# Optimization experiments

Measured on AMD Instinct MI355X. Metric: run time of the kernel, lower is better.

The kernel has to match this reference:

```python
import jax, jax.numpy as jnp
import numpy as np

N, H, D = 4, 8, 256          # num_layers, num_heads, hid_dim
DK = D // H                  # 32
DFF = D * 2                  # 512
B, L = 4, 2048               # batch, max_len


def _init_proj(key, shape):
    # matches torch init: uniform(-scale, scale), scale = sqrt(6/(fan_in+fan_out))
    s = float(np.sqrt(6.0 / (shape[-1] + shape[-2])))
    return jax.random.uniform(key, shape, jnp.float32, -s, s)


def setup_inputs() -> dict:
    key = jax.random.key(0)
    ks = jax.random.split(key, 8)
    x = jax.random.normal(ks[0], (B, L, D), jnp.float32)
    mask = (jax.random.uniform(ks[1], (B, L)) < 0.9).astype(jnp.float32)
    return {
        "x": x,
        "mask": mask,
        "Wq": _init_proj(ks[2], (N, H, D, DK)),
        "Wk": _init_proj(ks[3], (N, H, D, DK)),
        "Wv": _init_proj(ks[4], (N, H, D, DK)),
        "Wo": _init_proj(ks[5], (N, DK * H, D)),
        "W1": _init_proj(ks[6], (N, D, DFF)),
        "b1": jnp.zeros((N, 1, 1, DFF), jnp.float32),
        "W2": _init_proj(ks[7], (N, DFF, D)),
        "b2": jnp.zeros((N, 1, 1, D), jnp.float32),
    }


def reference(x, mask, Wq, Wk, Wv, Wo, W1, b1, W2, b2):
    b, l, d = x.shape
    neg = jnp.finfo(x.dtype).min
    m2 = mask[:, :, None] * mask[:, None, :]          # [b,l,l]
    layer_mask = (1.0 - m2)[:, None, :, :] * neg       # [b,1,l,l]

    def layer(xc, p):
        wq, wk, wv, wo, w1, bb1, w2, bb2 = p
        q = jnp.einsum('bld,hde->bhle', xc, wq)
        k = jnp.einsum('bld,hde->bhle', xc, wk)
        v = jnp.einsum('bld,hde->bhle', xc, wv)
        # NOTE: no 1/sqrt(dk) scaling in the original module
        A = jax.nn.softmax(jnp.einsum('bhle,bhke->bhlk', q, k) + layer_mask, axis=-1)
        # original contracts A (labeled bhkl) over l -> effectively A^T @ v
        o = jnp.einsum('bhkl,bhle->bkhe', A, v).reshape(b, l, d)
        xc = (o @ wo + xc) * 0.5
        ff = jax.nn.gelu(xc @ w1 + bb1, approximate=False)  # exact erf gelu, as torch F.gelu
        ff = ff @ w2 + bb2
        return (ff + xc) * 0.5, None

    out, _ = jax.lax.scan(layer, x, (Wq, Wk, Wv, Wo, W1, b1, W2, b2))
    return out
```

## Files before the change

kernel.cpp:

```cpp
#include <hip/hip_runtime.h>
#include <hip/hip_bf16.h>
#include <math.h>

#define NEGF (-3.402823466e38f)

typedef unsigned int u32;
typedef unsigned short u16;
typedef __attribute__((ext_vector_type(8))) short s16x8;
typedef __attribute__((ext_vector_type(4))) float f32x4;

#define MFMA16(a, b, c) __builtin_amdgcn_mfma_f32_16x16x32_bf16(a, b, c, 0, 0, 0)

__device__ __forceinline__ u32 pkhi(float a, float b) {
  return __builtin_amdgcn_perm(__builtin_bit_cast(u32, b),
                               __builtin_bit_cast(u32, a), 0x07060302u);
}
__device__ __forceinline__ float bftrunc(float x) {
  return __builtin_bit_cast(float, __builtin_bit_cast(u32, x) & 0xFFFF0000u);
}

__global__ void prep_wqkv_kernel(const float* __restrict__ Wq,
                                 const float* __restrict__ Wk,
                                 const float* __restrict__ Wv,
                                 float* __restrict__ WT) {
  int idx = blockIdx.x * 256 + threadIdx.x;
  const int total = 4 * 256 * 768;
  if (idx >= total) return;
  int col = idx % 768;
  int d   = (idx / 768) % 256;
  int n   = idx / (768 * 256);
  int ty  = col >> 8;
  int h   = (col >> 5) & 7;
  int e   = col & 31;
  const float* W = (ty == 0) ? Wq : (ty == 1) ? Wk : Wv;
  WT[idx] = W[(((size_t)n * 8 + h) * 256 + d) * 32 + e];
}

template <int EP>
__global__ __launch_bounds__(256)
void gemm_f32_kernel(const float* __restrict__ A, const float* __restrict__ B,
                     float* __restrict__ C, const float* __restrict__ bias,
                     const float* __restrict__ res, u16* __restrict__ Ch,
                     u16* __restrict__ Cl, int M, int N, int K) {
  __shared__ float As[128][36];
  __shared__ float Bs[32][64];
  const int t  = threadIdx.x;
  const int r0 = blockIdx.x * 128;
  const int n0 = blockIdx.y * 64;
  const int tc = t & 15;
  const int tr = t >> 4;

  float acc[8][4];
  #pragma unroll
  for (int j = 0; j < 8; ++j)
    #pragma unroll
    for (int c = 0; c < 4; ++c) acc[j][c] = 0.f;

  for (int k0 = 0; k0 < K; k0 += 32) {
    __syncthreads();
    #pragma unroll
    for (int i = 0; i < 4; ++i) {
      int e = t + 256 * i;
      int row = e >> 3, kq = e & 7;
      float4 f = *(const float4*)(A + (size_t)(r0 + row) * K + k0 + kq * 4);
      *(float4*)&As[row][kq * 4] = f;
    }
    #pragma unroll
    for (int i = 0; i < 2; ++i) {
      int e = t + 256 * i;
      int row = e >> 4, cq = e & 15;
      float4 f = *(const float4*)(B + (size_t)(k0 + row) * N + n0 + cq * 4);
      *(float4*)&Bs[row][cq * 4] = f;
    }
    __syncthreads();
    #pragma unroll
    for (int kk = 0; kk < 32; ++kk) {
      float bfrag[4];
      *(float4*)bfrag = *(const float4*)&Bs[kk][tc * 4];
      float afrag[8];
      #pragma unroll
      for (int j = 0; j < 8; ++j) afrag[j] = As[tr + 16 * j][kk];
      #pragma unroll
      for (int j = 0; j < 8; ++j)
        #pragma unroll
        for (int c = 0; c < 4; ++c) acc[j][c] += afrag[j] * bfrag[c];
    }
  }

  #pragma unroll
  for (int j = 0; j < 8; ++j) {
    int row = r0 + tr + 16 * j;
    size_t off = (size_t)row * N + n0 + tc * 4;
    float xa[4];
    #pragma unroll
    for (int c = 0; c < 4; ++c) {
      float x = acc[j][c];
      if (EP == 1) {
        x += bias[n0 + tc * 4 + c];
        x = 0.5f * x * (1.f + erff(x * 0.70710678118654752f));
      } else if (EP == 2) {
        if (bias) x += bias[n0 + tc * 4 + c];
        x = (x + res[off + c]) * 0.5f;
      }
      xa[c] = x;
    }
    if (EP == 3) {
      u32 h01 = pkhi(xa[0], xa[1]), h23 = pkhi(xa[2], xa[3]);
      u32 l01 = pkhi(xa[0] - bftrunc(xa[0]), xa[1] - bftrunc(xa[1]));
      u32 l23 = pkhi(xa[2] - bftrunc(xa[2]), xa[3] - bftrunc(xa[3]));
      *(uint2*)(Ch + off) = make_uint2(h01, h23);
      *(uint2*)(Cl + off) = make_uint2(l01, l23);
    } else {
      *(float4*)(C + off) = make_float4(xa[0], xa[1], xa[2], xa[3]);
    }
  }
}

__global__ __launch_bounds__(256)
void vtrans_kernel(const u16* __restrict__ qh, const u16* __restrict__ ql,
                   u16* __restrict__ vth, u16* __restrict__ vtl) {
  __shared__ u16 T[128][36];
  const int wg = blockIdx.x;
  const int tb = wg & 15, h = (wg >> 4) & 7, b = wg >> 7;
  const int t = threadIdx.x;
  const int tok = t >> 1, eo = (t & 1) * 16;
  const int e = t >> 3, seg = t & 7;
  #pragma unroll 1
  for (int pass = 0; pass < 2; ++pass) {
    const u16* src = pass ? ql : qh;
    u16* dst = pass ? vtl : vth;
    if (pass) __syncthreads();
    const u16* p = src + (size_t)(b * 2048 + tb * 128 + tok) * 768 + 512 + h * 32 + eo;
    uint2 u0 = *(const uint2*)p;
    uint2 u1 = *(const uint2*)(p + 4);
    uint2 u2 = *(const uint2*)(p + 8);
    uint2 u3 = *(const uint2*)(p + 12);
    *(uint2*)&T[tok][eo]      = u0;
    *(uint2*)&T[tok][eo + 4]  = u1;
    *(uint2*)&T[tok][eo + 8]  = u2;
    *(uint2*)&T[tok][eo + 12] = u3;
    __syncthreads();
    u32 w[8];
    #pragma unroll
    for (int i = 0; i < 8; ++i) {
      u32 lo16 = T[seg * 16 + 2 * i][e];
      u32 hi16 = T[seg * 16 + 2 * i + 1][e];
      w[i] = lo16 | (hi16 << 16);
    }
    u16* q = dst + ((size_t)((b * 8 + h) * 32 + e)) * 2048 + tb * 128 + seg * 16;
    *(uint4*)q       = make_uint4(w[0], w[1], w[2], w[3]);
    *(uint4*)(q + 8) = make_uint4(w[4], w[5], w[6], w[7]);
  }
}

__global__ __launch_bounds__(64)
void attn_mfma_kernel(const u16* __restrict__ qh, const u16* __restrict__ ql,
                      const u16* __restrict__ vth, const u16* __restrict__ vtl,
                      const float* __restrict__ mask, float* __restrict__ out) {
  __shared__ u16 PH[16][40];
  __shared__ u16 PL[16][40];
  const int wg = blockIdx.x;
  const int bh = wg & 31, qt = wg >> 5;
  const int b = bh >> 3, h = bh & 7;
  const int bL = b * 2048;
  const int lane = threadIdx.x;
  const int q = lane & 15, g = lane >> 4;

  const size_t qoff = (size_t)(bL + qt * 16 + q) * 768 + h * 32 + g * 8;
  const s16x8 Qh  = *(const s16x8*)(qh + qoff);
  const s16x8 Qlo = *(const s16x8*)(ql + qoff);
  const float mq = mask[bL + qt * 16 + q];

  const u16* kb_h = qh + (size_t)(bL + q) * 768 + 256 + h * 32 + g * 8;
  const u16* kb_l = ql + (size_t)(bL + q) * 768 + 256 + h * 32 + g * 8;
  const u16* vb_h0 = vth + ((size_t)(bh * 32 + q)) * 2048 + g * 8;
  const u16* vb_h1 = vth + ((size_t)(bh * 32 + 16 + q)) * 2048 + g * 8;
  const u16* vb_l0 = vtl + ((size_t)(bh * 32 + q)) * 2048 + g * 8;
  const u16* vb_l1 = vtl + ((size_t)(bh * 32 + 16 + q)) * 2048 + g * 8;
  const float* mb = mask + bL + (lane & 31);

  f32x4 Oa = {}, Ob = {};
  float m = NEGF, l = 0.f;

  #pragma unroll 1
  for (int t = 0; t < 64; ++t) {
    const size_t ko = (size_t)t * 32 * 768;
    const s16x8 K0h = *(const s16x8*)(kb_h + ko);
    const s16x8 K1h = *(const s16x8*)(kb_h + ko + 16 * 768);
    const s16x8 K0l = *(const s16x8*)(kb_l + ko);
    const s16x8 K1l = *(const s16x8*)(kb_l + ko + 16 * 768);
    const s16x8 V0h = *(const s16x8*)(vb_h0 + t * 32);
    const s16x8 V1h = *(const s16x8*)(vb_h1 + t * 32);
    const s16x8 V0l = *(const s16x8*)(vb_l0 + t * 32);
    const s16x8 V1l = *(const s16x8*)(vb_l1 + t * 32);
    const float mk = mb[t * 32];

    f32x4 S0 = {}, S1 = {};
    S0 = MFMA16(K0h, Qh,  S0);  S1 = MFMA16(K1h, Qh,  S1);
    S0 = MFMA16(K0l, Qh,  S0);  S1 = MFMA16(K1l, Qh,  S1);
    S0 = MFMA16(K0h, Qlo, S0);  S1 = MFMA16(K1h, Qlo, S1);

    u32 em = (u32)__ballot(mk != 0.f);
    em = (mq != 0.f) ? em : 0u;
    float se[8];
    #pragma unroll
    for (int r = 0; r < 4; ++r) {
      se[r]     = ((em >> (g * 4 + r)) & 1u)      ? S0[r] : NEGF;
      se[4 + r] = ((em >> (16 + g * 4 + r)) & 1u) ? S1[r] : NEGF;
    }
    float mt = fmaxf(fmaxf(fmaxf(se[0], se[1]), fmaxf(se[2], se[3])),
                     fmaxf(fmaxf(se[4], se[5]), fmaxf(se[6], se[7])));
    mt = fmaxf(mt, __shfl_xor(mt, 16));
    mt = fmaxf(mt, __shfl_xor(mt, 32));
    const float mn = fmaxf(m, mt);
    const float rr = __expf(m - mn);
    l *= rr;
    #pragma unroll
    for (int r = 0; r < 4; ++r) { Oa[r] *= rr; Ob[r] *= rr; }
    m = mn;
    float p[8];
    #pragma unroll
    for (int r = 0; r < 8; ++r) p[r] = __expf(fminf(se[r] - m, 60.f));
    l += (((p[0] + p[1]) + (p[2] + p[3])) + ((p[4] + p[5]) + (p[6] + p[7])));

    u32 ph0 = pkhi(p[0], p[1]), ph1 = pkhi(p[2], p[3]);
    u32 ph2 = pkhi(p[4], p[5]), ph3 = pkhi(p[6], p[7]);
    u32 pl0 = pkhi(p[0] - bftrunc(p[0]), p[1] - bftrunc(p[1]));
    u32 pl1 = pkhi(p[2] - bftrunc(p[2]), p[3] - bftrunc(p[3]));
    u32 pl2 = pkhi(p[4] - bftrunc(p[4]), p[5] - bftrunc(p[5]));
    u32 pl3 = pkhi(p[6] - bftrunc(p[6]), p[7] - bftrunc(p[7]));
    *(uint2*)&PH[q][g * 4]      = make_uint2(ph0, ph1);
    *(uint2*)&PH[q][16 + g * 4] = make_uint2(ph2, ph3);
    *(uint2*)&PL[q][g * 4]      = make_uint2(pl0, pl1);
    *(uint2*)&PL[q][16 + g * 4] = make_uint2(pl2, pl3);
    const s16x8 Pw  = *(const s16x8*)&PH[q][g * 8];
    const s16x8 Pwl = *(const s16x8*)&PL[q][g * 8];

    Oa = MFMA16(V0h, Pw,  Oa);  Ob = MFMA16(V1h, Pw,  Ob);
    Oa = MFMA16(V0l, Pw,  Oa);  Ob = MFMA16(V1l, Pw,  Ob);
    Oa = MFMA16(V0h, Pwl, Oa);  Ob = MFMA16(V1h, Pwl, Ob);
  }

  l += __shfl_xor(l, 16);
  l += __shfl_xor(l, 32);
  const float inv = 1.f / fmaxf(l, 1e-30f);

  float* op = out + (size_t)(bL + qt * 16 + q) * 256 + h * 32;
  *(float4*)(op + g * 4) =
      make_float4(Oa[0] * inv, Oa[1] * inv, Oa[2] * inv, Oa[3] * inv);
  *(float4*)(op + 16 + g * 4) =
      make_float4(Ob[0] * inv, Ob[1] * inv, Ob[2] * inv, Ob[3] * inv);
}

extern "C" void kernel_launch(void* const* d_in, const int* in_sizes, int n_in,
                              void* d_out, int out_size, void* d_ws, size_t ws_size,
                              hipStream_t stream) {
  const float* x    = (const float*)d_in[0];
  const float* mask = (const float*)d_in[1];
  const float* Wq   = (const float*)d_in[2];
  const float* Wk   = (const float*)d_in[3];
  const float* Wv   = (const float*)d_in[4];
  const float* Wo   = (const float*)d_in[5];
  const float* W1   = (const float*)d_in[6];
  const float* b1   = (const float*)d_in[7];
  const float* W2   = (const float*)d_in[8];
  const float* b2   = (const float*)d_in[9];
  float* outp = (float*)d_out;

  char* ws = (char*)d_ws;
  float* xc    = (float*)(ws);
  u16*   qh    = (u16*)(ws + ((size_t)8  << 20));
  u16*   ql    = (u16*)(ws + ((size_t)20 << 20));
  u16*   vth   = (u16*)(ws + ((size_t)32 << 20));
  u16*   vtl   = (u16*)(ws + ((size_t)36 << 20));
  float* wqkvT = (float*)(ws + ((size_t)40 << 20));
  float* ffb   = (float*)(ws + ((size_t)8  << 20));
  float* attno = outp;

  hipMemcpyAsync(xc, x, (size_t)8192 * 256 * sizeof(float),
                 hipMemcpyDeviceToDevice, stream);
  prep_wqkv_kernel<<<3072, 256, 0, stream>>>(Wq, Wk, Wv, wqkvT);

  for (int n = 0; n < 4; ++n) {
    gemm_f32_kernel<3><<<dim3(64, 12), 256, 0, stream>>>(
        xc, wqkvT + (size_t)n * 256 * 768, nullptr, nullptr, nullptr,
        qh, ql, 8192, 768, 256);
    vtrans_kernel<<<512, 256, 0, stream>>>(qh, ql, vth, vtl);
    attn_mfma_kernel<<<4096, 64, 0, stream>>>(qh, ql, vth, vtl, mask, attno);
    gemm_f32_kernel<2><<<dim3(64, 4), 256, 0, stream>>>(
        attno, Wo + (size_t)n * 256 * 256, xc, nullptr, xc, nullptr, nullptr,
        8192, 256, 256);
    gemm_f32_kernel<1><<<dim3(64, 8), 256, 0, stream>>>(
        xc, W1 + (size_t)n * 256 * 512, ffb, b1 + (size_t)n * 512, nullptr,
        nullptr, nullptr, 8192, 512, 256);
    gemm_f32_kernel<2><<<dim3(64, 4), 256, 0, stream>>>(
        ffb, W2 + (size_t)n * 512 * 256, (n == 3) ? outp : xc,
        b2 + (size_t)n * 256, xc, nullptr, nullptr, 8192, 256, 512);
  }
}
```

Baseline: 1.596 ms.

## Move projection and FFN GEMMs to split-bf16 MFMA and widen attention tiles

Replaces the scalar fp32 GEMMs with MFMA GEMMs that use a three-term hi/lo bf16 split. Weights are pre-split and transposed per layer by a new prep kernel, and intermediate activations (attention output, FFN hidden) are stored as hi/lo bf16 pairs. The attention kernel now runs four waves per block, processes 64 keys per iteration, and skips the running-max rescale unless the max grows by more than a threshold. The goal is to remove the vector-ALU GEMM cost and cut loop overhead in attention. The cost is extra per-layer weight-prep launches, and the attention output buffer is aliased onto d_out.

```diff
diff --git a/kernel.cpp b/kernel.cpp
--- a/kernel.cpp
+++ b/kernel.cpp
@@ -18,102 +18,175 @@
 __device__ __forceinline__ float bftrunc(float x) {
   return __builtin_bit_cast(float, __builtin_bit_cast(u32, x) & 0xFFFF0000u);
 }
-
-__global__ void prep_wqkv_kernel(const float* __restrict__ Wq,
-                                 const float* __restrict__ Wk,
-                                 const float* __restrict__ Wv,
-                                 float* __restrict__ WT) {
-  int idx = blockIdx.x * 256 + threadIdx.x;
-  const int total = 4 * 256 * 768;
-  if (idx >= total) return;
-  int col = idx % 768;
-  int d   = (idx / 768) % 256;
-  int n   = idx / (768 * 256);
-  int ty  = col >> 8;
-  int h   = (col >> 5) & 7;
-  int e   = col & 31;
-  const float* W = (ty == 0) ? Wq : (ty == 1) ? Wk : Wv;
-  WT[idx] = W[(((size_t)n * 8 + h) * 256 + d) * 32 + e];
-}
-
-template <int EP>
+__device__ __forceinline__ u16 hib(float x) {
+  return (u16)(__builtin_bit_cast(u32, x) >> 16);
+}
+
 __global__ __launch_bounds__(256)
-void gemm_f32_kernel(const float* __restrict__ A, const float* __restrict__ B,
-                     float* __restrict__ C, const float* __restrict__ bias,
-                     const float* __restrict__ res, u16* __restrict__ Ch,
-                     u16* __restrict__ Cl, int M, int N, int K) {
-  __shared__ float As[128][36];
-  __shared__ float Bs[32][64];
-  const int t  = threadIdx.x;
-  const int r0 = blockIdx.x * 128;
-  const int n0 = blockIdx.y * 64;
-  const int tc = t & 15;
-  const int tr = t >> 4;
-
-  float acc[8][4];
-  #pragma unroll
-  for (int j = 0; j < 8; ++j)
-    #pragma unroll
-    for (int c = 0; c < 4; ++c) acc[j][c] = 0.f;
+void wprep_kernel(const float* __restrict__ Wq, const float* __restrict__ Wk,
+                  const float* __restrict__ Wv, const float* __restrict__ Wo,
+                  const float* __restrict__ W1, const float* __restrict__ W2,
+                  int layer,
+                  u16* __restrict__ qkvh, u16* __restrict__ qkvl,
+                  u16* __restrict__ woh, u16* __restrict__ wol,
+                  u16* __restrict__ w1h, u16* __restrict__ w1l,
+                  u16* __restrict__ w2h, u16* __restrict__ w2l) {
+  __shared__ float L[32][33];
+  const int b = blockIdx.x, t = threadIdx.x;
+  const float* src; int spitch; u16 *dh, *dl; int dpitch;
+  if (b < 192) {
+    int ty = b / 64, rem = b % 64, h = rem >> 3, dt = rem & 7;
+    const float* W = (ty == 0) ? Wq : (ty == 1) ? Wk : Wv;
+    src = W + (((size_t)layer * 8 + h) * 256 + dt * 32) * 32;
+    spitch = 32;
+    dh = qkvh + (size_t)(ty * 256 + h * 32) * 256 + dt * 32;
+    dl = qkvl + (size_t)(ty * 256 + h * 32) * 256 + dt * 32;
+    dpitch = 256;
+  } else if (b < 256) {
+    int b2 = b - 192, kt = b2 >> 3, nt = b2 & 7;
+    src = Wo + (size_t)layer * 65536 + (size_t)(kt * 32) * 256 + nt * 32;
+    spitch = 256;
+    dh = woh + (size_t)(nt * 32) * 256 + kt * 32;
+    dl = wol + (size_t)(nt * 32) * 256 + kt * 32;
+    dpitch = 256;
+  } else if (b < 384) {
+    int b3 = b - 256, kt = b3 >> 4, nt = b3 & 15;
+    src = W1 + (size_t)layer * 131072 + (size_t)(kt * 32) * 512 + nt * 32;
+    spitch = 512;
+    dh = w1h + (size_t)(nt * 32) * 256 + kt * 32;
+    dl = w1l + (size_t)(nt * 32) * 256 + kt * 32;
+    dpitch = 256;
+  } else {
+    int b4 = b - 384, kt = b4 >> 3, nt = b4 & 7;
+    src = W2 + (size_t)layer * 131072 + (size_t)(kt * 32) * 256 + nt * 32;
+    spitch = 256;
+    dh = w2h + (size_t)(nt * 32) * 512 + kt * 32;
+    dl = w2l + (size_t)(nt * 32) * 512 + kt * 32;
+    dpitch = 512;
+  }
+  {
+    int kk = t >> 3, n4 = (t & 7) * 4;
+    float4 f = *(const float4*)(src + (size_t)kk * spitch + n4);
+    L[kk][n4] = f.x; L[kk][n4 + 1] = f.y; L[kk][n4 + 2] = f.z; L[kk][n4 + 3] = f.w;
+  }
+  __syncthreads();
+  {
+    int nn = t >> 3, k4 = (t & 7) * 4;
+    float x0 = L[k4][nn], x1 = L[k4 + 1][nn], x2 = L[k4 + 2][nn], x3 = L[k4 + 3][nn];
+    *(uint2*)(dh + (size_t)nn * dpitch + k4) = make_uint2(pkhi(x0, x1), pkhi(x2, x3));
+    float l0 = x0 - bftrunc(x0), l1 = x1 - bftrunc(x1);
+    float l2 = x2 - bftrunc(x2), l3 = x3 - bftrunc(x3);
+    *(uint2*)(dl + (size_t)nn * dpitch + k4) = make_uint2(pkhi(l0, l1), pkhi(l2, l3));
+  }
+}
+
+template <int AMODE, int EP>
+__global__ __launch_bounds__(256)
+void gemm_mfma_kernel(const float* __restrict__ Af,
+                      const u16* __restrict__ Ahp, const u16* __restrict__ Alp,
+                      const u16* __restrict__ BTh, const u16* __restrict__ BTl,
+                      float* __restrict__ Cf, u16* __restrict__ Chp,
+                      u16* __restrict__ Clp, const float* __restrict__ bias,
+                      const float* __restrict__ res, int M, int N, int K) {
+  __shared__ u16 Ah[128][40], Al[128][40], Bh[64][40], Bl[64][40];
+  const int t = threadIdx.x;
+  const int wave = t >> 6, lane = t & 63;
+  const int q = lane & 15, g = lane >> 4;
+  const int wr = wave >> 1, wc = wave & 1;
+  const int r0 = blockIdx.x * 128, n0 = blockIdx.y * 64;
+
+  f32x4 acc[4][2] = {};
 
   for (int k0 = 0; k0 < K; k0 += 32) {
     __syncthreads();
-    #pragma unroll
-    for (int i = 0; i < 4; ++i) {
-      int e = t + 256 * i;
-      int row = e >> 3, kq = e & 7;
-      float4 f = *(const float4*)(A + (size_t)(r0 + row) * K + k0 + kq * 4);
-      *(float4*)&As[row][kq * 4] = f;
-    }
-    #pragma unroll
-    for (int i = 0; i < 2; ++i) {
-      int e = t + 256 * i;
-      int row = e >> 4, cq = e & 15;
-      float4 f = *(const float4*)(B + (size_t)(k0 + row) * N + n0 + cq * 4);
-      *(float4*)&Bs[row][cq * 4] = f;
+    {
+      int row = t >> 1, half = t & 1;
+      if (AMODE == 0) {
+        const float* src = Af + (size_t)(r0 + row) * K + k0 + half * 16;
+        float xv[16];
+        #pragma unroll
+        for (int i = 0; i < 4; ++i) {
+          float4 f = *(const float4*)(src + 4 * i);
+          xv[4*i] = f.x; xv[4*i+1] = f.y; xv[4*i+2] = f.z; xv[4*i+3] = f.w;
+        }
+        uint4 H0 = make_uint4(pkhi(xv[0], xv[1]), pkhi(xv[2], xv[3]),
+                              pkhi(xv[4], xv[5]), pkhi(xv[6], xv[7]));
+        uint4 H1 = make_uint4(pkhi(xv[8], xv[9]), pkhi(xv[10], xv[11]),
+                              pkhi(xv[12], xv[13]), pkhi(xv[14], xv[15]));
+        float rv[16];
+        #pragma unroll
+        for (int i = 0; i < 16; ++i) rv[i] = xv[i] - bftrunc(xv[i]);
+        uint4 L0 = make_uint4(pkhi(rv[0], rv[1]), pkhi(rv[2], rv[3]),
+                              pkhi(rv[4], rv[5]), pkhi(rv[6], rv[7]));
+        uint4 L1 = make_uint4(pkhi(rv[8], rv[9]), pkhi(rv[10], rv[11]),
+                              pkhi(rv[12], rv[13]), pkhi(rv[14], rv[15]));
+        *(uint4*)&Ah[row][half * 16]     = H0;
+        *(uint4*)&Ah[row][half * 16 + 8] = H1;
+        *(uint4*)&Al[row][half * 16]     = L0;
+        *(uint4*)&Al[row][half * 16 + 8] = L1;
+      } else {
+        const u16* sh = Ahp + (size_t)(r0 + row) * K + k0 + half * 16;
+        const u16* sl = Alp + (size_t)(r0 + row) * K + k0 + half * 16;
+        *(uint4*)&Ah[row][half * 16]     = *(const uint4*)sh;
+        *(uint4*)&Ah[row][half * 16 + 8] = *(const uint4*)(sh + 8);
+        *(uint4*)&Al[row][half * 16]     = *(const uint4*)sl;
+        *(uint4*)&Al[row][half * 16 + 8] = *(const uint4*)(sl + 8);
+      }
+    }
+    {
+      int n = t >> 2, seg = t & 3;
+      size_t off = (size_t)(n0 + n) * K + k0 + seg * 8;
+      *(uint4*)&Bh[n][seg * 8] = *(const uint4*)(BTh + off);
+      *(uint4*)&Bl[n][seg * 8] = *(const uint4*)(BTl + off);
     }
     __syncthreads();
-    #pragma unroll
-    for (int kk = 0; kk < 32; ++kk) {
-      float bfrag[4];
-      *(float4*)bfrag = *(const float4*)&Bs[kk][tc * 4];
-      float afrag[8];
+
+    s16x8 afh[4], afl[4], bfh[2], bfl[2];
+    #pragma unroll
+    for (int mi = 0; mi < 4; ++mi) {
+      afh[mi] = *(const s16x8*)&Ah[wr * 64 + mi * 16 + q][g * 8];
+      afl[mi] = *(const s16x8*)&Al[wr * 64 + mi * 16 + q][g * 8];
+    }
+    #pragma unroll
+    for (int nj = 0; nj < 2; ++nj) {
+      bfh[nj] = *(const s16x8*)&Bh[wc * 32 + nj * 16 + q][g * 8];
+      bfl[nj] = *(const s16x8*)&Bl[wc * 32 + nj * 16 + q][g * 8];
+    }
+    #pragma unroll
+    for (int mi = 0; mi < 4; ++mi)
       #pragma unroll
-      for (int j = 0; j < 8; ++j) afrag[j] = As[tr + 16 * j][kk];
+      for (int nj = 0; nj < 2; ++nj) {
+        acc[mi][nj] = MFMA16(afh[mi], bfh[nj], acc[mi][nj]);
+        acc[mi][nj] = MFMA16(afl[mi], bfh[nj], acc[mi][nj]);
+        acc[mi][nj] = MFMA16(afh[mi], bfl[nj], acc[mi][nj]);
+      }
+  }
+
+  #pragma unroll
+  for (int mi = 0; mi < 4; ++mi)
+    #pragma unroll
+    for (int nj = 0; nj < 2; ++nj) {
+      const int col = n0 + wc * 32 + nj * 16 + q;
       #pragma unroll
-      for (int j = 0; j < 8; ++j)
-        #pragma unroll
-        for (int c = 0; c < 4; ++c) acc[j][c] += afrag[j] * bfrag[c];
-    }
-  }
-
-  #pragma unroll
-  for (int j = 0; j < 8; ++j) {
-    int row = r0 + tr + 16 * j;
-    size_t off = (size_t)row * N + n0 + tc * 4;
-    float xa[4];
-    #pragma unroll
-    for (int c = 0; c < 4; ++c) {
-      float x = acc[j][c];
-      if (EP == 1) {
-        x += bias[n0 + tc * 4 + c];
-        x = 0.5f * x * (1.f + erff(x * 0.70710678118654752f));
-      } else if (EP == 2) {
-        if (bias) x += bias[n0 + tc * 4 + c];
-        x = (x + res[off + c]) * 0.5f;
+      for (int r = 0; r < 4; ++r) {
+        const int row = r0 + wr * 64 + mi * 16 + g * 4 + r;
+        const size_t off = (size_t)row * N + col;
+        float x = acc[mi][nj][r];
+        if (EP == 1) {
+          x += bias[col];
+          x = 0.5f * x * (1.f + erff(x * 0.70710678118654752f));
+        } else if (EP == 2) {
+          if (bias) x += bias[col];
+          x = (x + res[off]) * 0.5f;
+        }
+        if (EP == 2) {
+          Cf[off] = x;
+        } else {
+          Chp[off] = hib(x);
+          Clp[off] = hib(x - bftrunc(x));
+        }
       }
-      xa[c] = x;
-    }
-    if (EP == 3) {
-      u32 h01 = pkhi(xa[0], xa[1]), h23 = pkhi(xa[2], xa[3]);
-      u32 l01 = pkhi(xa[0] - bftrunc(xa[0]), xa[1] - bftrunc(xa[1]));
-      u32 l23 = pkhi(xa[2] - bftrunc(xa[2]), xa[3] - bftrunc(xa[3]));
-      *(uint2*)(Ch + off) = make_uint2(h01, h23);
-      *(uint2*)(Cl + off) = make_uint2(l01, l23);
-    } else {
-      *(float4*)(C + off) = make_float4(xa[0], xa[1], xa[2], xa[3]);
-    }
-  }
+    }
 }
 
 __global__ __launch_bounds__(256)
@@ -147,109 +220,138 @@
       u32 hi16 = T[seg * 16 + 2 * i + 1][e];
       w[i] = lo16 | (hi16 << 16);
     }
-    u16* q = dst + ((size_t)((b * 8 + h) * 32 + e)) * 2048 + tb * 128 + seg * 16;
-    *(uint4*)q       = make_uint4(w[0], w[1], w[2], w[3]);
-    *(uint4*)(q + 8) = make_uint4(w[4], w[5], w[6], w[7]);
-  }
-}
-
-__global__ __launch_bounds__(64)
+    u16* qp = dst + ((size_t)((b * 8 + h) * 32 + e)) * 2048 + tb * 128 + seg * 16;
+    *(uint4*)qp       = make_uint4(w[0], w[1], w[2], w[3]);
+    *(uint4*)(qp + 8) = make_uint4(w[4], w[5], w[6], w[7]);
+  }
+}
+
+__global__ __launch_bounds__(256, 4)
 void attn_mfma_kernel(const u16* __restrict__ qh, const u16* __restrict__ ql,
                       const u16* __restrict__ vth, const u16* __restrict__ vtl,
-                      const float* __restrict__ mask, float* __restrict__ out) {
-  __shared__ u16 PH[16][40];
-  __shared__ u16 PL[16][40];
+                      const float* __restrict__ mask,
+                      u16* __restrict__ oh, u16* __restrict__ ol) {
+  __shared__ u16 PH[4][16][72];
+  __shared__ u16 PL[4][16][72];
   const int wg = blockIdx.x;
-  const int bh = wg & 31, qt = wg >> 5;
+  const int bh = wg & 31, qtg = wg >> 5;
   const int b = bh >> 3, h = bh & 7;
   const int bL = b * 2048;
-  const int lane = threadIdx.x;
+  const int t = threadIdx.x;
+  const int wave = t >> 6, lane = t & 63;
   const int q = lane & 15, g = lane >> 4;
+  const int qt = qtg * 4 + wave;
 
   const size_t qoff = (size_t)(bL + qt * 16 + q) * 768 + h * 32 + g * 8;
   const s16x8 Qh  = *(const s16x8*)(qh + qoff);
   const s16x8 Qlo = *(const s16x8*)(ql + qoff);
   const float mq = mask[bL + qt * 16 + q];
 
-  const u16* kb_h = qh + (size_t)(bL + q) * 768 + 256 + h * 32 + g * 8;
-  const u16* kb_l = ql + (size_t)(bL + q) * 768 + 256 + h * 32 + g * 8;
-  const u16* vb_h0 = vth + ((size_t)(bh * 32 + q)) * 2048 + g * 8;
-  const u16* vb_h1 = vth + ((size_t)(bh * 32 + 16 + q)) * 2048 + g * 8;
-  const u16* vb_l0 = vtl + ((size_t)(bh * 32 + q)) * 2048 + g * 8;
-  const u16* vb_l1 = vtl + ((size_t)(bh * 32 + 16 + q)) * 2048 + g * 8;
-  const float* mb = mask + bL + (lane & 31);
+  const u16* kb_h = qh + ((size_t)(bL + q) * 768 + 256 + h * 32 + g * 8);
+  const u16* kb_l = ql + ((size_t)(bL + q) * 768 + 256 + h * 32 + g * 8);
+  const u16* vb_h = vth + (size_t)(bh * 32 + q) * 2048 + g * 8;
+  const u16* vb_l = vtl + (size_t)(bh * 32 + q) * 2048 + g * 8;
+  const float* mb = mask + bL + lane;
 
   f32x4 Oa = {}, Ob = {};
   float m = NEGF, l = 0.f;
 
   #pragma unroll 1
-  for (int t = 0; t < 64; ++t) {
-    const size_t ko = (size_t)t * 32 * 768;
-    const s16x8 K0h = *(const s16x8*)(kb_h + ko);
-    const s16x8 K1h = *(const s16x8*)(kb_h + ko + 16 * 768);
-    const s16x8 K0l = *(const s16x8*)(kb_l + ko);
-    const s16x8 K1l = *(const s16x8*)(kb_l + ko + 16 * 768);
-    const s16x8 V0h = *(const s16x8*)(vb_h0 + t * 32);
-    const s16x8 V1h = *(const s16x8*)(vb_h1 + t * 32);
-    const s16x8 V0l = *(const s16x8*)(vb_l0 + t * 32);
-    const s16x8 V1l = *(const s16x8*)(vb_l1 + t * 32);
-    const float mk = mb[t * 32];
-
-    f32x4 S0 = {}, S1 = {};
-    S0 = MFMA16(K0h, Qh,  S0);  S1 = MFMA16(K1h, Qh,  S1);
-    S0 = MFMA16(K0l, Qh,  S0);  S1 = MFMA16(K1l, Qh,  S1);
-    S0 = MFMA16(K0h, Qlo, S0);  S1 = MFMA16(K1h, Qlo, S1);
-
-    u32 em = (u32)__ballot(mk != 0.f);
-    em = (mq != 0.f) ? em : 0u;
-    float se[8];
+  for (int tt = 0; tt < 32; ++tt) {
+    const size_t kof = (size_t)tt * 64 * 768;
+    const s16x8 K0h = *(const s16x8*)(kb_h + kof);
+    const s16x8 K1h = *(const s16x8*)(kb_h + kof + 16 * 768);
+    const s16x8 K2h = *(const s16x8*)(kb_h + kof + 32 * 768);
+    const s16x8 K3h = *(const s16x8*)(kb_h + kof + 48 * 768);
+    const s16x8 K0l = *(const s16x8*)(kb_l + kof);
+    const s16x8 K1l = *(const s16x8*)(kb_l + kof + 16 * 768);
+    const s16x8 K2l = *(const s16x8*)(kb_l + kof + 32 * 768);
+    const s16x8 K3l = *(const s16x8*)(kb_l + kof + 48 * 768);
+    const float mk = mb[tt * 64];
+
+    f32x4 S0 = {}, S1 = {}, S2 = {}, S3 = {};
+    S0 = MFMA16(K0h, Qh, S0);  S1 = MFMA16(K1h, Qh, S1);
+    S2 = MFMA16(K2h, Qh, S2);  S3 = MFMA16(K3h, Qh, S3);
+    S0 = MFMA16(K0l, Qh, S0);  S1 = MFMA16(K1l, Qh, S1);
+    S2 = MFMA16(K2l, Qh, S2);  S3 = MFMA16(K3l, Qh, S3);
+    S0 = MFMA16(K0h, Qlo, S0); S1 = MFMA16(K1h, Qlo, S1);
+    S2 = MFMA16(K2h, Qlo, S2); S3 = MFMA16(K3h, Qlo, S3);
+
+    const int vo = tt * 64;
+    const s16x8 Vah  = *(const s16x8*)(vb_h + vo);
+    const s16x8 Vbh  = *(const s16x8*)(vb_h + vo + 32);
+    const s16x8 V1ah = *(const s16x8*)(vb_h + 16 * 2048 + vo);
+    const s16x8 V1bh = *(const s16x8*)(vb_h + 16 * 2048 + vo + 32);
+    const s16x8 Val  = *(const s16x8*)(vb_l + vo);
+    const s16x8 Vbl  = *(const s16x8*)(vb_l + vo + 32);
+    const s16x8 V1al = *(const s16x8*)(vb_l + 16 * 2048 + vo);
+    const s16x8 V1bl = *(const s16x8*)(vb_l + 16 * 2048 + vo + 32);
+
+    unsigned long long em = __ballot(mk != 0.f);
+    em = (mq != 0.f) ? em : 0ull;
+    float p[16];
     #pragma unroll
     for (int r = 0; r < 4; ++r) {
-      se[r]     = ((em >> (g * 4 + r)) & 1u)      ? S0[r] : NEGF;
-      se[4 + r] = ((em >> (16 + g * 4 + r)) & 1u) ? S1[r] : NEGF;
-    }
-    float mt = fmaxf(fmaxf(fmaxf(se[0], se[1]), fmaxf(se[2], se[3])),
-                     fmaxf(fmaxf(se[4], se[5]), fmaxf(se[6], se[7])));
+      p[r]      = ((em >> (g * 4 + r)) & 1ull)      ? S0[r] : NEGF;
+      p[4 + r]  = ((em >> (16 + g * 4 + r)) & 1ull) ? S1[r] : NEGF;
+      p[8 + r]  = ((em >> (32 + g * 4 + r)) & 1ull) ? S2[r] : NEGF;
+      p[12 + r] = ((em >> (48 + g * 4 + r)) & 1ull) ? S3[r] : NEGF;
+    }
+    float mt = fmaxf(fmaxf(fmaxf(p[0], p[1]), fmaxf(p[2], p[3])),
+                     fmaxf(fmaxf(p[4], p[5]), fmaxf(p[6], p[7])));
+    mt = fmaxf(mt, fmaxf(fmaxf(fmaxf(p[8], p[9]), fmaxf(p[10], p[11])),
+                         fmaxf(fmaxf(p[12], p[13]), fmaxf(p[14], p[15]))));
     mt = fmaxf(mt, __shfl_xor(mt, 16));
     mt = fmaxf(mt, __shfl_xor(mt, 32));
-    const float mn = fmaxf(m, mt);
-    const float rr = __expf(m - mn);
-    l *= rr;
-    #pragma unroll
-    for (int r = 0; r < 4; ++r) { Oa[r] *= rr; Ob[r] *= rr; }
-    m = mn;
-    float p[8];
-    #pragma unroll
-    for (int r = 0; r < 8; ++r) p[r] = __expf(fminf(se[r] - m, 60.f));
-    l += (((p[0] + p[1]) + (p[2] + p[3])) + ((p[4] + p[5]) + (p[6] + p[7])));
-
-    u32 ph0 = pkhi(p[0], p[1]), ph1 = pkhi(p[2], p[3]);
-    u32 ph2 = pkhi(p[4], p[5]), ph3 = pkhi(p[6], p[7]);
-    u32 pl0 = pkhi(p[0] - bftrunc(p[0]), p[1] - bftrunc(p[1]));
-    u32 pl1 = pkhi(p[2] - bftrunc(p[2]), p[3] - bftrunc(p[3]));
-    u32 pl2 = pkhi(p[4] - bftrunc(p[4]), p[5] - bftrunc(p[5]));
-    u32 pl3 = pkhi(p[6] - bftrunc(p[6]), p[7] - bftrunc(p[7]));
-    *(uint2*)&PH[q][g * 4]      = make_uint2(ph0, ph1);
-    *(uint2*)&PH[q][16 + g * 4] = make_uint2(ph2, ph3);
-    *(uint2*)&PL[q][g * 4]      = make_uint2(pl0, pl1);
-    *(uint2*)&PL[q][16 + g * 4] = make_uint2(pl2, pl3);
-    const s16x8 Pw  = *(const s16x8*)&PH[q][g * 8];
-    const s16x8 Pwl = *(const s16x8*)&PL[q][g * 8];
-
-    Oa = MFMA16(V0h, Pw,  Oa);  Ob = MFMA16(V1h, Pw,  Ob);
-    Oa = MFMA16(V0l, Pw,  Oa);  Ob = MFMA16(V1l, Pw,  Ob);
-    Oa = MFMA16(V0h, Pwl, Oa);  Ob = MFMA16(V1h, Pwl, Ob);
+    if (__any(mt > m + 8.f)) {
+      const float mn = fmaxf(m, mt);
+      const float rr = __expf(m - mn);
+      l *= rr;
+      #pragma unroll
+      for (int r = 0; r < 4; ++r) { Oa[r] *= rr; Ob[r] *= rr; }
+      m = mn;
+    }
+    #pragma unroll
+    for (int j = 0; j < 16; ++j) p[j] = __expf(fminf(p[j] - m, 60.f));
+    l += (((p[0] + p[1]) + (p[2] + p[3])) + ((p[4] + p[5]) + (p[6] + p[7])))
+       + (((p[8] + p[9]) + (p[10] + p[11])) + ((p[12] + p[13]) + (p[14] + p[15])));
+
+    #pragma unroll
+    for (int i = 0; i < 4; ++i) {
+      float a0 = p[4*i], a1 = p[4*i+1], a2 = p[4*i+2], a3 = p[4*i+3];
+      *(uint2*)&PH[wave][q][i * 16 + g * 4] =
+          make_uint2(pkhi(a0, a1), pkhi(a2, a3));
+      float l0 = a0 - bftrunc(a0), l1 = a1 - bftrunc(a1);
+      float l2 = a2 - bftrunc(a2), l3 = a3 - bftrunc(a3);
+      *(uint2*)&PL[wave][q][i * 16 + g * 4] =
+          make_uint2(pkhi(l0, l1), pkhi(l2, l3));
+    }
+    const s16x8 Pah = *(const s16x8*)&PH[wave][q][g * 8];
+    const s16x8 Pbh = *(const s16x8*)&PH[wave][q][32 + g * 8];
+    const s16x8 Pal = *(const s16x8*)&PL[wave][q][g * 8];
+    const s16x8 Pbl = *(const s16x8*)&PL[wave][q][32 + g * 8];
+
+    Oa = MFMA16(Vah, Pah, Oa);  Oa = MFMA16(Val, Pah, Oa);  Oa = MFMA16(Vah, Pal, Oa);
+    Oa = MFMA16(Vbh, Pbh, Oa);  Oa = MFMA16(Vbl, Pbh, Oa);  Oa = MFMA16(Vbh, Pbl, Oa);
+    Ob = MFMA16(V1ah, Pah, Ob); Ob = MFMA16(V1al, Pah, Ob); Ob = MFMA16(V1ah, Pal, Ob);
+    Ob = MFMA16(V1bh, Pbh, Ob); Ob = MFMA16(V1bl, Pbh, Ob); Ob = MFMA16(V1bh, Pbl, Ob);
   }
 
   l += __shfl_xor(l, 16);
   l += __shfl_xor(l, 32);
   const float inv = 1.f / fmaxf(l, 1e-30f);
 
-  float* op = out + (size_t)(bL + qt * 16 + q) * 256 + h * 32;
-  *(float4*)(op + g * 4) =
-      make_float4(Oa[0] * inv, Oa[1] * inv, Oa[2] * inv, Oa[3] * inv);
-  *(float4*)(op + 16 + g * 4) =
-      make_float4(Ob[0] * inv, Ob[1] * inv, Ob[2] * inv, Ob[3] * inv);
+  const size_t ob = (size_t)(bL + qt * 16 + q) * 256 + h * 32;
+  float a0 = Oa[0] * inv, a1 = Oa[1] * inv, a2 = Oa[2] * inv, a3 = Oa[3] * inv;
+  float b0 = Ob[0] * inv, b1 = Ob[1] * inv, b2 = Ob[2] * inv, b3 = Ob[3] * inv;
+  *(uint2*)&oh[ob + g * 4]      = make_uint2(pkhi(a0, a1), pkhi(a2, a3));
+  *(uint2*)&oh[ob + 16 + g * 4] = make_uint2(pkhi(b0, b1), pkhi(b2, b3));
+  float ra0 = a0 - bftrunc(a0), ra1 = a1 - bftrunc(a1);
+  float ra2 = a2 - bftrunc(a2), ra3 = a3 - bftrunc(a3);
+  float rb0 = b0 - bftrunc(b0), rb1 = b1 - bftrunc(b1);
+  float rb2 = b2 - bftrunc(b2), rb3 = b3 - bftrunc(b3);
+  *(uint2*)&ol[ob + g * 4]      = make_uint2(pkhi(ra0, ra1), pkhi(ra2, ra3));
+  *(uint2*)&ol[ob + 16 + g * 4] = make_uint2(pkhi(rb0, rb1), pkhi(rb2, rb3));
 }
 
 extern "C" void kernel_launch(void* const* d_in, const int* in_sizes, int n_in,
@@ -268,33 +370,46 @@
   float* outp = (float*)d_out;
 
   char* ws = (char*)d_ws;
-  float* xc    = (float*)(ws);
-  u16*   qh    = (u16*)(ws + ((size_t)8  << 20));
-  u16*   ql    = (u16*)(ws + ((size_t)20 << 20));
-  u16*   vth   = (u16*)(ws + ((size_t)32 << 20));
-  u16*   vtl   = (u16*)(ws + ((size_t)36 << 20));
-  float* wqkvT = (float*)(ws + ((size_t)40 << 20));
-  float* ffb   = (float*)(ws + ((size_t)8  << 20));
-  float* attno = outp;
+  float* xc  = (float*)(ws);
+  u16*   qh  = (u16*)(ws + ((size_t)8  << 20));
+  u16*   ql  = (u16*)(ws + ((size_t)20 << 20));
+  u16*   vth = (u16*)(ws + ((size_t)32 << 20));
+  u16*   vtl = (u16*)(ws + ((size_t)36 << 20));
+  char* wb = ws + ((size_t)40 << 20);
+  u16* qkvTh = (u16*)(wb);
+  u16* qkvTl = (u16*)(wb + 393216);
+  u16* woTh  = (u16*)(wb + 786432);
+  u16* woTl  = (u16*)(wb + 917504);
+  u16* w1Th  = (u16*)(wb + 1048576);
+  u16* w1Tl  = (u16*)(wb + 1310720);
+  u16* w2Th  = (u16*)(wb + 1572864);
+  u16* w2Tl  = (u16*)(wb + 1835008);
+  u16* ffh = qh;
+  u16* ffl = ql;
+  u16* attnoh = (u16*)d_out;
+  u16* attnol = attnoh + (size_t)8192 * 256;
 
   hipMemcpyAsync(xc, x, (size_t)8192 * 256 * sizeof(float),
                  hipMemcpyDeviceToDevice, stream);
-  prep_wqkv_kernel<<<3072, 256, 0, stream>>>(Wq, Wk, Wv, wqkvT);
 
   for (int n = 0; n < 4; ++n) {
-    gemm_f32_kernel<3><<<dim3(64, 12), 256, 0, stream>>>(
-        xc, wqkvT + (size_t)n * 256 * 768, nullptr, nullptr, nullptr,
-        qh, ql, 8192, 768, 256);
+    wprep_kernel<<<512, 256, 0, stream>>>(Wq, Wk, Wv, Wo, W1, W2, n,
+                                          qkvTh, qkvTl, woTh, woTl,
+                                          w1Th, w1Tl, w2Th, w2Tl);
+    gemm_mfma_kernel<0, 0><<<dim3(64, 12), 256, 0, stream>>>(
+        xc, nullptr, nullptr, qkvTh, qkvTl, nullptr, qh, ql,
+        nullptr, nullptr, 8192, 768, 256);
     vtrans_kernel<<<512, 256, 0, stream>>>(qh, ql, vth, vtl);
-    attn_mfma_kernel<<<4096, 64, 0, stream>>>(qh, ql, vth, vtl, mask, attno);
-    gemm_f32_kernel<2><<<dim3(64, 4), 256, 0, stream>>>(
-        attno, Wo + (size_t)n * 256 * 256, xc, nullptr, xc, nullptr, nullptr,
-        8192, 256, 256);
-    gemm_f32_kernel<1><<<dim3(64, 8), 256, 0, stream>>>(
-        xc, W1 + (size_t)n * 256 * 512, ffb, b1 + (size_t)n * 512, nullptr,
-        nullptr, nullptr, 8192, 512, 256);
-    gemm_f32_kernel<2><<<dim3(64, 4), 256, 0, stream>>>(
-        ffb, W2 + (size_t)n * 512 * 256, (n == 3) ? outp : xc,
-        b2 + (size_t)n * 256, xc, nullptr, nullptr, 8192, 256, 512);
-  }
-}
+    attn_mfma_kernel<<<1024, 256, 0, stream>>>(qh, ql, vth, vtl, mask,
+                                               attnoh, attnol);
+    gemm_mfma_kernel<1, 2><<<dim3(64, 4), 256, 0, stream>>>(
+        nullptr, attnoh, attnol, woTh, woTl, xc, nullptr, nullptr,
+        nullptr, xc, 8192, 256, 256);
+    gemm_mfma_kernel<0, 1><<<dim3(64, 8), 256, 0, stream>>>(
+        xc, nullptr, nullptr, w1Th, w1Tl, nullptr, ffh, ffl,
+        b1 + (size_t)n * 512, nullptr, 8192, 512, 256);
+    gemm_mfma_kernel<1, 2><<<dim3(64, 4), 256, 0, stream>>>(
+        nullptr, ffh, ffl, w2Th, w2Tl, (n == 3) ? outp : xc, nullptr, nullptr,
+        b2 + (size_t)n * 256, xc, 8192, 256, 512);
+  }
+}
```

Result: faster. 1.342 ms (-15.9%).
